# Optimization experiments

Hardware: AMD Instinct MI355X
Metric: run time of the kernel (lower is better)

The kernel has to match this reference:

```python
import jax, jax.numpy as jnp
import numpy as np

N_EMBD = 1024
N_HEAD = 16
HEAD_DIM = N_EMBD // N_HEAD
SCALE = HEAD_DIM ** -0.5


def setup_inputs() -> dict:
    key = jax.random.key(0)
    ks = jax.random.split(key, 6)
    B, T = 64, 256
    s = N_EMBD ** -0.5
    return {
        "x": jax.random.normal(ks[0], (B, T, N_EMBD), dtype=jnp.float32),
        "Wq": jax.random.normal(ks[1], (N_EMBD, N_EMBD), dtype=jnp.float32) * s,
        "Wk": jax.random.normal(ks[2], (N_EMBD, N_EMBD), dtype=jnp.float32) * s,
        "Wv": jax.random.normal(ks[3], (N_EMBD, N_EMBD), dtype=jnp.float32) * s,
        "Wo": jax.random.normal(ks[4], (N_EMBD, N_EMBD), dtype=jnp.float32) * s,
        "bo": jax.random.normal(ks[5], (N_EMBD,), dtype=jnp.float32) * 0.01,
    }


def reference(x, Wq, Wk, Wv, Wo, bo):
    B, T, C = x.shape
    # QKV projections (no bias), split heads -> [B, H, T, Dh]
    def heads(y):
        return y.reshape(B, T, N_HEAD, HEAD_DIM).transpose(0, 2, 1, 3)
    q = heads(x @ Wq)
    k = heads(x @ Wk)
    v = heads(x @ Wv)
    # scaled causal attention scores [B, H, T, T]
    wei = jnp.einsum("bhqd,bhkd->bhqk", q, k) * SCALE
    causal = jnp.tril(jnp.ones((T, T), dtype=bool))
    wei = jnp.where(causal, wei, -jnp.inf)
    wei = jax.nn.softmax(wei, axis=-1)
    # dropout is identity in eval mode
    out = jnp.einsum("bhqk,bhkd->bhqd", wei, v)
    out = out.transpose(0, 2, 1, 3).reshape(B, T, C)
    return out @ Wo + bo
```

## Files before the change

### kernel.cpp

```cpp
#include <hip/hip_runtime.h>
#include <hip/hip_bf16.h>
#include <stdint.h>

typedef __attribute__((ext_vector_type(8))) short bfx8;
typedef __attribute__((ext_vector_type(4))) short bfx4;
typedef __attribute__((ext_vector_type(4))) float f32x4;
typedef __attribute__((ext_vector_type(4))) unsigned short us4;

#define SCALE_ATT 0.125f

__device__ __forceinline__ unsigned short f2bf(float f) {
  union { float f; unsigned u; } a; a.f = f;
  unsigned r = a.u + 0x7fffu + ((a.u >> 16) & 1u);
  return (unsigned short)(r >> 16);
}

__device__ __forceinline__ void gll16(const void* g, void* l) {
  __builtin_amdgcn_global_load_lds(
      (__attribute__((address_space(1))) void*)(g),
      (__attribute__((address_space(3))) void*)(l), 16, 0, 0);
}

__device__ __forceinline__ bfx8 ld2x64(const unsigned short* p) {
  bfx4 lo = *(const bfx4*)p;
  bfx4 hi = *(const bfx4*)(p + 4);
  return __builtin_shufflevector(lo, hi, 0, 1, 2, 3, 4, 5, 6, 7);
}

__global__ __launch_bounds__(256) void cvt_x(const float* __restrict__ x,
                                             unsigned short* __restrict__ xb, int n4) {
  int i = blockIdx.x * blockDim.x + threadIdx.x;
  int stride = gridDim.x * blockDim.x;
  const float4* x4 = (const float4*)x;
  for (; i < n4; i += stride) {
    float4 v = x4[i];
    us4 o;
    o[0] = f2bf(v.x); o[1] = f2bf(v.y); o[2] = f2bf(v.z); o[3] = f2bf(v.w);
    *(us4*)&xb[(size_t)i * 4] = o;
  }
}

__global__ __launch_bounds__(256) void cvt_w(const float* __restrict__ W0, const float* __restrict__ W1,
                                             const float* __restrict__ W2, const float* __restrict__ W3,
                                             unsigned short* __restrict__ T0, unsigned short* __restrict__ T1,
                                             unsigned short* __restrict__ T2, unsigned short* __restrict__ T3) {
  const float* W; unsigned short* T;
  switch (blockIdx.z) {
    case 0: W = W0; T = T0; break;
    case 1: W = W1; T = T1; break;
    case 2: W = W2; T = T2; break;
    default: W = W3; T = T3; break;
  }
  __shared__ unsigned short Ts[64][68];
  int k0 = blockIdx.x * 64, n0 = blockIdx.y * 64;
  int t = threadIdx.x;
  int lrow = t >> 4, c4 = t & 15;
  #pragma unroll
  for (int i = 0; i < 4; i++) {
    int row = lrow + i * 16;
    float4 v = *(const float4*)&W[(size_t)(k0 + row) * 1024 + n0 + c4 * 4];
    Ts[c4 * 4 + 0][row] = f2bf(v.x);
    Ts[c4 * 4 + 1][row] = f2bf(v.y);
    Ts[c4 * 4 + 2][row] = f2bf(v.z);
    Ts[c4 * 4 + 3][row] = f2bf(v.w);
  }
  __syncthreads();
  int f = t >> 5, sub = t & 31;
  int nt_l = f >> 1, ks_l = f & 1;
  size_t base = ((size_t)(((n0 >> 4) + nt_l) * 32 + (k0 >> 5) + ks_l)) * 512;
  #pragma unroll
  for (int i = 0; i < 2; i++) {
    int l = sub * 2 + i;
    int row = nt_l * 16 + (l & 15);
    int col = ks_l * 32 + ((l >> 4) << 3);
    us4 a = *(const us4*)&Ts[row][col];
    us4 b = *(const us4*)&Ts[row][col + 4];
    *(us4*)&T[base + l * 8] = a;
    *(us4*)&T[base + l * 8 + 4] = b;
  }
}

#define DS_BAR() __builtin_amdgcn_s_barrier()
#define SB0() __builtin_amdgcn_sched_barrier(0)
#define LGKM(N) do { asm volatile("s_waitcnt lgkmcnt(" #N ")" ::: "memory"); SB0(); } while (0)
#define VMW(N) do { asm volatile("s_waitcnt vmcnt(" #N ")" ::: "memory"); SB0(); } while (0)

#define STAGE(hs, gb, r0, kbyte) do { \
  const char* _g = (const char*)(gb) + (size_t)((r0) + srow) * 2048 + (size_t)(kbyte) + scolb; \
  gll16(_g, (hs) + w * 1024); \
  gll16(_g + 16 * 2048, (hs) + w * 1024 + 512); \
} while (0)

#define LOADA(dst, ptr, qm) \
  _Pragma("unroll") for (int mi = 0; mi < 4; ++mi) \
    dst[mi] = *(const bfx8*)&(ptr)[(wm * 128 + (qm) * 64 + mi * 16 + lr) * 32 + rcol];

#define LOADBG(dst, ks) \
  _Pragma("unroll") for (int ni = 0; ni < 4; ++ni) \
    dst[ni] = *(const bfx8*)&Bpw[((size_t)(ni * 32 + (ks))) * 512];

#define MFMA16(rb, a, b) \
  _Pragma("unroll") for (int mi = 0; mi < 4; ++mi) \
    _Pragma("unroll") for (int ni = 0; ni < 4; ++ni) \
      acc[(rb) + mi][ni] = __builtin_amdgcn_mfma_f32_16x16x32_bf16(a[mi], b[ni], acc[(rb) + mi][ni], 0, 0, 0);

template<int MODE>
__global__ __launch_bounds__(512, 2) void gemm8p(
    const unsigned short* __restrict__ A,
    const unsigned short* __restrict__ Bt0, const unsigned short* __restrict__ Bt1,
    const unsigned short* __restrict__ Bt2,
    unsigned short* __restrict__ O0, unsigned short* __restrict__ O1,
    unsigned short* __restrict__ O2,
    const float* __restrict__ bias, float* __restrict__ OutF, int nby) {
  __shared__ unsigned short A0s[2][256 * 32];
  __shared__ unsigned short A1s[2][256 * 32];

  int tid = threadIdx.x;
  int w = tid >> 6, l = tid & 63;
  int lr = l & 15, lh = l >> 4;
  int wm = w >> 2, wn = w & 3;
  int srow = w * 32 + (l >> 2);
  int scolb = ((l & 3) * 16) ^ (((l >> 5) & 1) << 5);
  int rcol = (lh * 8) ^ (((lr >> 3) & 1) << 4);

  int cpx = gridDim.x >> 3;
  int o = blockIdx.x;
  int wg = (o & 7) * cpx + (o >> 3);
  int bm = wg / nby, bn = wg % nby;

  const unsigned short* Bt;
  unsigned short* Ob = nullptr;
  int n0;
  if (MODE == 0) {
    int sel = bn >> 2;
    n0 = (bn & 3) * 256;
    Bt = sel == 0 ? Bt0 : (sel == 1 ? Bt1 : Bt2);
    Ob = sel == 0 ? O0 : (sel == 1 ? O1 : O2);
  } else {
    Bt = Bt0;
    n0 = bn * 256;
  }
  int am0 = bm * 256;
  const unsigned short* Bpw = Bt + ((size_t)((n0 >> 4) + wn * 4) * 32) * 512 + (size_t)l * 8;

  f32x4 acc[8][4];
  #pragma unroll
  for (int i = 0; i < 8; ++i)
    #pragma unroll
    for (int jj = 0; jj < 4; ++jj) acc[i][jj] = (f32x4){0.f, 0.f, 0.f, 0.f};

  bfx8 af[4], ag[4], b0[4], b1[4];

  STAGE(A0s[0], A, am0, 0);   STAGE(A1s[0], A, am0, 64);  SB0();
  LOADBG(b0, 0); SB0();
  LOADBG(b1, 1); SB0();
  VMW(8);
  DS_BAR();

  int cur = 0;
  #pragma unroll 1
  for (int t = 0; t < 15; ++t) {
    int kb = (t + 1) * 128;
    int ks2 = (t + 1) * 2;
    unsigned short* A0c = A0s[cur];       unsigned short* A1c = A1s[cur];
    unsigned short* A0n = A0s[cur ^ 1];   unsigned short* A1n = A1s[cur ^ 1];
    LOADA(af, A0c, 0);  LOADA(ag, A0c, 1);  SB0();
    STAGE(A0n, A, am0, kb);  STAGE(A1n, A, am0, kb + 64);  SB0();
    LGKM(4); VMW(8);
    __builtin_amdgcn_s_setprio(1);  MFMA16(0, af, b0);
    __builtin_amdgcn_s_setprio(0);
    LGKM(0);
    __builtin_amdgcn_s_setprio(1);  MFMA16(4, ag, b0);
    __builtin_amdgcn_s_setprio(0);
    LOADBG(b0, ks2); SB0();
    LOADA(af, A1c, 0);  LOADA(ag, A1c, 1);  SB0();
    LGKM(4); VMW(8);
    __builtin_amdgcn_s_setprio(1);  MFMA16(0, af, b1);
    __builtin_amdgcn_s_setprio(0);
    LGKM(0);
    __builtin_amdgcn_s_setprio(1);  MFMA16(4, ag, b1);
    __builtin_amdgcn_s_setprio(0);
    LOADBG(b1, ks2 + 1); SB0();
    VMW(8);
    DS_BAR();
    cur ^= 1;
  }
  LOADA(af, A0s[1], 0);  LOADA(ag, A0s[1], 1);  SB0();
  LGKM(4); VMW(4);
  __builtin_amdgcn_s_setprio(1);  MFMA16(0, af, b0);
  __builtin_amdgcn_s_setprio(0);
  LGKM(0);
  __builtin_amdgcn_s_setprio(1);  MFMA16(4, ag, b0);
  __builtin_amdgcn_s_setprio(0);
  LOADA(af, A1s[1], 0);  LOADA(ag, A1s[1], 1);  SB0();
  LGKM(4); VMW(0);
  __builtin_amdgcn_s_setprio(1);  MFMA16(0, af, b1);
  __builtin_amdgcn_s_setprio(0);
  LGKM(0);
  __builtin_amdgcn_s_setprio(1);  MFMA16(4, ag, b1);
  __builtin_amdgcn_s_setprio(0);

  float bv[4];
  if (MODE == 1) {
    #pragma unroll
    for (int ni = 0; ni < 4; ++ni) bv[ni] = bias[n0 + wn * 64 + ni * 16 + lr];
  }
  #pragma unroll
  for (int mi8 = 0; mi8 < 8; ++mi8)
    #pragma unroll
    for (int ni = 0; ni < 4; ++ni)
      #pragma unroll
      for (int j = 0; j < 4; ++j) {
        int r = am0 + wm * 128 + mi8 * 16 + lh * 4 + j;
        int c = n0 + wn * 64 + ni * 16 + lr;
        if (MODE == 0)
          Ob[(size_t)r * 1024 + c] = f2bf(acc[mi8][ni][j]);
        else
          OutF[(size_t)r * 1024 + c] = acc[mi8][ni][j] + bv[ni];
      }
}

__global__ __launch_bounds__(256, 4) void attn_kernel(
    const unsigned short* __restrict__ Qb, const unsigned short* __restrict__ Kb,
    const unsigned short* __restrict__ Vb, unsigned short* __restrict__ Ab) {
  __shared__ unsigned short Vt[64][260];
  __shared__ unsigned short Pw[4][16][36];

  int t = threadIdx.x;
  int w = t >> 6, l = t & 63;
  int lr = l & 15, lh = l >> 4;
  int bh = blockIdx.x;
  size_t rowbase = (size_t)(bh >> 4) * 256 * 1024 + (size_t)(bh & 15) * 64;

  {
    int rr = t >> 3, part = t & 7;
    for (int i = 0; i < 8; i++) {
      int row = i * 32 + rr;
      bfx8 vv = *(const bfx8*)(Vb + rowbase + (size_t)row * 1024 + part * 8);
      #pragma unroll
      for (int e = 0; e < 8; e++) Vt[part * 8 + e][row] = (unsigned short)vv[e];
    }
  }
  __syncthreads();

  for (int qt = 0; qt < 4; qt++) {
    int r0 = qt * 64 + w * 16;
    int rmax = r0 + 15;
    const unsigned short* Qrow = Qb + rowbase + (size_t)(r0 + lr) * 1024 + lh * 8;
    bfx8 aq0 = *(const bfx8*)(Qrow);
    bfx8 aq1 = *(const bfx8*)(Qrow + 32);

    float m[4], lsum[4];
    #pragma unroll
    for (int j = 0; j < 4; j++) { m[j] = -1e30f; lsum[j] = 0.f; }
    f32x4 oc[4];
    #pragma unroll
    for (int ct = 0; ct < 4; ct++) oc[ct] = (f32x4){0.f, 0.f, 0.f, 0.f};

    int nkc = (rmax >> 6) + 1;
    for (int kc = 0; kc < nkc; kc++) {
      int kbase = kc * 64;
      bool haveB = (kbase + 32) <= rmax;
      const unsigned short* Kr = Kb + rowbase + (size_t)(kbase + lr) * 1024 + lh * 8;

      bfx8 k0a = *(const bfx8*)(Kr);
      bfx8 k0b = *(const bfx8*)(Kr + 32);
      bfx8 k1a = *(const bfx8*)(Kr + 16 * 1024);
      bfx8 k1b = *(const bfx8*)(Kr + 16 * 1024 + 32);
      f32x4 s0 = (f32x4){0.f, 0.f, 0.f, 0.f};
      f32x4 s1 = (f32x4){0.f, 0.f, 0.f, 0.f};
      f32x4 s2 = (f32x4){0.f, 0.f, 0.f, 0.f};
      f32x4 s3 = (f32x4){0.f, 0.f, 0.f, 0.f};
      __builtin_amdgcn_s_setprio(1);
      s0 = __builtin_amdgcn_mfma_f32_16x16x32_bf16(aq0, k0a, s0, 0, 0, 0);
      s0 = __builtin_amdgcn_mfma_f32_16x16x32_bf16(aq1, k0b, s0, 0, 0, 0);
      s1 = __builtin_amdgcn_mfma_f32_16x16x32_bf16(aq0, k1a, s1, 0, 0, 0);
      s1 = __builtin_amdgcn_mfma_f32_16x16x32_bf16(aq1, k1b, s1, 0, 0, 0);
      __builtin_amdgcn_s_setprio(0);
      if (haveB) {
        bfx8 k2a = *(const bfx8*)(Kr + 32 * 1024);
        bfx8 k2b = *(const bfx8*)(Kr + 32 * 1024 + 32);
        bfx8 k3a = *(const bfx8*)(Kr + 48 * 1024);
        bfx8 k3b = *(const bfx8*)(Kr + 48 * 1024 + 32);
        __builtin_amdgcn_s_setprio(1);
        s2 = __builtin_amdgcn_mfma_f32_16x16x32_bf16(aq0, k2a, s2, 0, 0, 0);
        s2 = __builtin_amdgcn_mfma_f32_16x16x32_bf16(aq1, k2b, s2, 0, 0, 0);
        s3 = __builtin_amdgcn_mfma_f32_16x16x32_bf16(aq0, k3a, s3, 0, 0, 0);
        s3 = __builtin_amdgcn_mfma_f32_16x16x32_bf16(aq1, k3b, s3, 0, 0, 0);
        __builtin_amdgcn_s_setprio(0);
      }

      int c0 = kbase + lr, c1 = c0 + 16, c2 = c0 + 32, c3 = c0 + 48;
      unsigned pb[4];
      #pragma unroll
      for (int j = 0; j < 4; j++) {
        int row = r0 + lh * 4 + j;
        float v0 = (c0 <= row) ? s0[j] : -1e30f;
        float v1 = (c1 <= row) ? s1[j] : -1e30f;
        float v2 = (c2 <= row) ? s2[j] : -1e30f;
        float v3 = (c3 <= row) ? s3[j] : -1e30f;
        float cm = fmaxf(fmaxf(v0, v1), fmaxf(v2, v3));
        cm = fmaxf(cm, __shfl_xor(cm, 1));
        cm = fmaxf(cm, __shfl_xor(cm, 2));
        cm = fmaxf(cm, __shfl_xor(cm, 4));
        cm = fmaxf(cm, __shfl_xor(cm, 8));
        float mn = fmaxf(m[j], cm);
        float sc = __expf((m[j] - mn) * SCALE_ATT);
        float p0 = (c0 <= row) ? __expf((s0[j] - mn) * SCALE_ATT) : 0.f;
        float p1 = (c1 <= row) ? __expf((s1[j] - mn) * SCALE_ATT) : 0.f;
        float p2 = (c2 <= row) ? __expf((s2[j] - mn) * SCALE_ATT) : 0.f;
        float p3 = (c3 <= row) ? __expf((s3[j] - mn) * SCALE_ATT) : 0.f;
        m[j] = mn;
        float cs = (p0 + p1) + (p2 + p3);
        cs += __shfl_xor(cs, 1);
        cs += __shfl_xor(cs, 2);
        cs += __shfl_xor(cs, 4);
        cs += __shfl_xor(cs, 8);
        lsum[j] = lsum[j] * sc + cs;
        #pragma unroll
        for (int ct = 0; ct < 4; ct++) oc[ct][j] *= sc;
        Pw[w][lh * 4 + j][lr] = f2bf(p0);
        Pw[w][lh * 4 + j][16 + lr] = f2bf(p1);
        pb[j] = (unsigned)f2bf(p2) | ((unsigned)f2bf(p3) << 16);
      }

      {
        bfx8 pa = ld2x64(&Pw[w][lr][lh * 8]);
        __builtin_amdgcn_s_setprio(1);
        #pragma unroll
        for (int ct = 0; ct < 4; ct++) {
          bfx8 vb = ld2x64(&Vt[ct * 16 + lr][kbase + lh * 8]);
          oc[ct] = __builtin_amdgcn_mfma_f32_16x16x32_bf16(pa, vb, oc[ct], 0, 0, 0);
        }
        __builtin_amdgcn_s_setprio(0);
      }
      if (haveB) {
        #pragma unroll
        for (int j = 0; j < 4; j++) {
          Pw[w][lh * 4 + j][lr] = (unsigned short)(pb[j] & 0xffffu);
          Pw[w][lh * 4 + j][16 + lr] = (unsigned short)(pb[j] >> 16);
        }
        bfx8 pa = ld2x64(&Pw[w][lr][lh * 8]);
        __builtin_amdgcn_s_setprio(1);
        #pragma unroll
        for (int ct = 0; ct < 4; ct++) {
          bfx8 vb = ld2x64(&Vt[ct * 16 + lr][kbase + 32 + lh * 8]);
          oc[ct] = __builtin_amdgcn_mfma_f32_16x16x32_bf16(pa, vb, oc[ct], 0, 0, 0);
        }
        __builtin_amdgcn_s_setprio(0);
      }
    }

    float rinv[4];
    #pragma unroll
    for (int j = 0; j < 4; j++) rinv[j] = 1.0f / lsum[j];
    #pragma unroll
    for (int ct = 0; ct < 4; ct++)
      #pragma unroll
      for (int j = 0; j < 4; j++) {
        int row = r0 + lh * 4 + j;
        Ab[rowbase + (size_t)row * 1024 + ct * 16 + lr] = f2bf(oc[ct][j] * rinv[j]);
      }
  }
}

extern "C" void kernel_launch(void* const* d_in, const int* in_sizes, int n_in,
                              void* d_out, int out_size, void* d_ws, size_t ws_size,
                              hipStream_t stream) {
  const float* x  = (const float*)d_in[0];
  const float* Wq = (const float*)d_in[1];
  const float* Wk = (const float*)d_in[2];
  const float* Wv = (const float*)d_in[3];
  const float* Wo = (const float*)d_in[4];
  const float* bo = (const float*)d_in[5];
  float* out = (float*)d_out;

  char* ws = (char*)d_ws;
  unsigned short* xb  = (unsigned short*)(ws);
  unsigned short* Wtq = (unsigned short*)(ws + (size_t)(32u << 20));
  unsigned short* Wtk = (unsigned short*)(ws + (size_t)(34u << 20));
  unsigned short* Wtv = (unsigned short*)(ws + (size_t)(36u << 20));
  unsigned short* Wto = (unsigned short*)(ws + (size_t)(38u << 20));
  unsigned short* Qb  = (unsigned short*)(ws + (size_t)(40u << 20));
  unsigned short* Kb  = (unsigned short*)(ws + (size_t)(72u << 20));
  unsigned short* Vb  = (unsigned short*)(ws + (size_t)(104u << 20));
  unsigned short* Ab  = xb;

  cvt_x<<<2048, 256, 0, stream>>>(x, xb, 4194304);
  cvt_w<<<dim3(16, 16, 4), 256, 0, stream>>>(Wq, Wk, Wv, Wo, Wtq, Wtk, Wtv, Wto);
  gemm8p<0><<<768, 512, 0, stream>>>(xb, Wtq, Wtk, Wtv, Qb, Kb, Vb, nullptr, nullptr, 12);
  attn_kernel<<<1024, 256, 0, stream>>>(Qb, Kb, Vb, Ab);
  gemm8p<1><<<256, 512, 0, stream>>>(Ab, Wto, Wto, Wto, nullptr, nullptr, nullptr, bo, out, 4);
}
```

Before: 207.3 us.

## Load GEMM A operand directly from global into registers, dropping LDS staging

Removes the LDS double-buffered staging of the A tile (global_load_lds, barriers, manual waitcnt) and instead has each wave load its A fragments directly from global memory into registers, software-pipelined with register double buffers like the B operand. This removes LDS traffic and block-wide barriers, but A rows are now fetched redundantly by the four waves sharing the same wm, which raises global/L2 traffic. It also relies on the compiler for wait scheduling instead of explicit sched barriers.

Result: slower. 354.6 us (+71.0%).

```diff
diff --git a/kernel.cpp b/kernel.cpp
--- a/kernel.cpp
+++ b/kernel.cpp
@@ -13,12 +13,6 @@
   union { float f; unsigned u; } a; a.f = f;
   unsigned r = a.u + 0x7fffu + ((a.u >> 16) & 1u);
   return (unsigned short)(r >> 16);
-}
-
-__device__ __forceinline__ void gll16(const void* g, void* l) {
-  __builtin_amdgcn_global_load_lds(
-      (__attribute__((address_space(1))) void*)(g),
-      (__attribute__((address_space(3))) void*)(l), 16, 0, 0);
 }
 
 __device__ __forceinline__ bfx8 ld2x64(const unsigned short* p) {
@@ -80,20 +74,9 @@
   }
 }
 
-#define DS_BAR() __builtin_amdgcn_s_barrier()
-#define SB0() __builtin_amdgcn_sched_barrier(0)
-#define LGKM(N) do { asm volatile("s_waitcnt lgkmcnt(" #N ")" ::: "memory"); SB0(); } while (0)
-#define VMW(N) do { asm volatile("s_waitcnt vmcnt(" #N ")" ::: "memory"); SB0(); } while (0)
-
-#define STAGE(hs, gb, r0, kbyte) do { \
-  const char* _g = (const char*)(gb) + (size_t)((r0) + srow) * 2048 + (size_t)(kbyte) + scolb; \
-  gll16(_g, (hs) + w * 1024); \
-  gll16(_g + 16 * 2048, (hs) + w * 1024 + 512); \
-} while (0)
-
-#define LOADA(dst, ptr, qm) \
+#define LOADAG(dst, qm, kel) \
   _Pragma("unroll") for (int mi = 0; mi < 4; ++mi) \
-    dst[mi] = *(const bfx8*)&(ptr)[(wm * 128 + (qm) * 64 + mi * 16 + lr) * 32 + rcol];
+    dst[mi] = *(const bfx8*)&Apw[(size_t)(((qm) * 64 + mi * 16) * 1024) + (kel)];
 
 #define LOADBG(dst, ks) \
   _Pragma("unroll") for (int ni = 0; ni < 4; ++ni) \
@@ -112,16 +95,10 @@
     unsigned short* __restrict__ O0, unsigned short* __restrict__ O1,
     unsigned short* __restrict__ O2,
     const float* __restrict__ bias, float* __restrict__ OutF, int nby) {
-  __shared__ unsigned short A0s[2][256 * 32];
-  __shared__ unsigned short A1s[2][256 * 32];
-
   int tid = threadIdx.x;
   int w = tid >> 6, l = tid & 63;
   int lr = l & 15, lh = l >> 4;
   int wm = w >> 2, wn = w & 3;
-  int srow = w * 32 + (l >> 2);
-  int scolb = ((l & 3) * 16) ^ (((l >> 5) & 1) << 5);
-  int rcol = (lh * 8) ^ (((lr >> 3) & 1) << 4);
 
   int cpx = gridDim.x >> 3;
   int o = blockIdx.x;
@@ -141,6 +118,7 @@
     n0 = bn * 256;
   }
   int am0 = bm * 256;
+  const unsigned short* Apw = A + (size_t)(am0 + wm * 128 + lr) * 1024 + lh * 8;
   const unsigned short* Bpw = Bt + ((size_t)((n0 >> 4) + wn * 4) * 32) * 512 + (size_t)l * 8;
 
   f32x4 acc[8][4];
@@ -149,55 +127,24 @@
     #pragma unroll
     for (int jj = 0; jj < 4; ++jj) acc[i][jj] = (f32x4){0.f, 0.f, 0.f, 0.f};
 
-  bfx8 af[4], ag[4], b0[4], b1[4];
-
-  STAGE(A0s[0], A, am0, 0);   STAGE(A1s[0], A, am0, 64);  SB0();
-  LOADBG(b0, 0); SB0();
-  LOADBG(b1, 1); SB0();
-  VMW(8);
-  DS_BAR();
-
-  int cur = 0;
+  bfx8 af[4], ag[4], af2[4], ag2[4], b0[4], b1[4];
+
+  LOADAG(af, 0, 0);  LOADAG(ag, 1, 0);  LOADBG(b0, 0);
+
   #pragma unroll 1
   for (int t = 0; t < 15; ++t) {
-    int kb = (t + 1) * 128;
-    int ks2 = (t + 1) * 2;
-    unsigned short* A0c = A0s[cur];       unsigned short* A1c = A1s[cur];
-    unsigned short* A0n = A0s[cur ^ 1];   unsigned short* A1n = A1s[cur ^ 1];
-    LOADA(af, A0c, 0);  LOADA(ag, A0c, 1);  SB0();
-    STAGE(A0n, A, am0, kb);  STAGE(A1n, A, am0, kb + 64);  SB0();
-    LGKM(4); VMW(8);
-    __builtin_amdgcn_s_setprio(1);  MFMA16(0, af, b0);
+    int kel = t * 64;
+    LOADAG(af2, 0, kel + 32);  LOADAG(ag2, 1, kel + 32);  LOADBG(b1, 2 * t + 1);
+    __builtin_amdgcn_s_setprio(1);  MFMA16(0, af, b0);  MFMA16(4, ag, b0);
     __builtin_amdgcn_s_setprio(0);
-    LGKM(0);
-    __builtin_amdgcn_s_setprio(1);  MFMA16(4, ag, b0);
+    LOADAG(af, 0, kel + 64);   LOADAG(ag, 1, kel + 64);  LOADBG(b0, 2 * t + 2);
+    __builtin_amdgcn_s_setprio(1);  MFMA16(0, af2, b1);  MFMA16(4, ag2, b1);
     __builtin_amdgcn_s_setprio(0);
-    LOADBG(b0, ks2); SB0();
-    LOADA(af, A1c, 0);  LOADA(ag, A1c, 1);  SB0();
-    LGKM(4); VMW(8);
-    __builtin_amdgcn_s_setprio(1);  MFMA16(0, af, b1);
-    __builtin_amdgcn_s_setprio(0);
-    LGKM(0);
-    __builtin_amdgcn_s_setprio(1);  MFMA16(4, ag, b1);
-    __builtin_amdgcn_s_setprio(0);
-    LOADBG(b1, ks2 + 1); SB0();
-    VMW(8);
-    DS_BAR();
-    cur ^= 1;
-  }
-  LOADA(af, A0s[1], 0);  LOADA(ag, A0s[1], 1);  SB0();
-  LGKM(4); VMW(4);
-  __builtin_amdgcn_s_setprio(1);  MFMA16(0, af, b0);
+  }
+  LOADAG(af2, 0, 15 * 64 + 32);  LOADAG(ag2, 1, 15 * 64 + 32);  LOADBG(b1, 31);
+  __builtin_amdgcn_s_setprio(1);  MFMA16(0, af, b0);   MFMA16(4, ag, b0);
   __builtin_amdgcn_s_setprio(0);
-  LGKM(0);
-  __builtin_amdgcn_s_setprio(1);  MFMA16(4, ag, b0);
-  __builtin_amdgcn_s_setprio(0);
-  LOADA(af, A1s[1], 0);  LOADA(ag, A1s[1], 1);  SB0();
-  LGKM(4); VMW(0);
-  __builtin_amdgcn_s_setprio(1);  MFMA16(0, af, b1);
-  __builtin_amdgcn_s_setprio(0);
-  LGKM(0);
-  __builtin_amdgcn_s_setprio(1);  MFMA16(4, ag, b1);
+  __builtin_amdgcn_s_setprio(1);  MFMA16(0, af2, b1);  MFMA16(4, ag2, b1);
   __builtin_amdgcn_s_setprio(0);
 
   float bv[4];
```
